# Kernel optimization log

Measured on AMD Instinct MI355X. Metric: run time of the kernel, lower is better.

Reference implementation:

```python
import jax, jax.numpy as jnp
import numpy as np

N = 10000   # nodes
E = 100000  # edges (before self-loops)
H = 4       # heads (layers 0-3); last layer uses 1 head
C = 200     # out_channels per head
IN_DIMS = [200, H * C, H * C, H * C, H * C]
HEADS   = [H, H, H, H, 1]
NEG_SLOPE = 0.2  # PyG GATConv default


def _gat_layer(x, src, dst, W, a_src, a_dst, b, heads):
    # x: [N, Fin], W: [Fin, heads*C], a_src/a_dst: [heads, C], b: [heads*C]
    h = (x @ W).reshape(N, heads, C)                       # [N,H,C]
    alpha_src = jnp.einsum('nhc,hc->nh', h, a_src)         # [N,H]
    alpha_dst = jnp.einsum('nhc,hc->nh', h, a_dst)         # [N,H]
    e = jax.nn.leaky_relu(alpha_src[src] + alpha_dst[dst], NEG_SLOPE)  # [E',H]
    # segment softmax over incoming edges of each dst node
    m = jax.ops.segment_max(e, dst, num_segments=N)        # [N,H]
    ex = jnp.exp(e - m[dst])                               # [E',H]
    den = jax.ops.segment_sum(ex, dst, num_segments=N)     # [N,H]
    alpha = ex / den[dst]                                  # [E',H]
    out = jax.ops.segment_sum(h[src] * alpha[:, :, None], dst, num_segments=N)
    return out.reshape(N, heads * C) + b, alpha


def setup_inputs() -> dict:
    key = jax.random.key(0)
    ks = jax.random.split(key, 2 + 4 * 5)
    inp = {}
    inp['X'] = jax.random.normal(ks[0], (N, 200), jnp.float32)
    inp['edge_index'] = jax.random.randint(ks[1], (2, E), 0, N, dtype=jnp.int32)
    k = 2
    for i in range(5):
        fin, hd = IN_DIMS[i], HEADS[i]
        s = 1.0 / np.sqrt(fin)
        inp[f'W{i}'] = jax.random.normal(ks[k], (fin, hd * C), jnp.float32) * s; k += 1
        inp[f'as{i}'] = jax.random.normal(ks[k], (hd, C), jnp.float32) * s; k += 1
        inp[f'ad{i}'] = jax.random.normal(ks[k], (hd, C), jnp.float32) * s; k += 1
        inp[f'b{i}'] = jnp.zeros((hd * C,), jnp.float32); k += 1
    return inp


def reference(X, edge_index,
              W0, as0, ad0, b0, W1, as1, ad1, b1, W2, as2, ad2, b2,
              W3, as3, ad3, b3, W4, as4, ad4, b4):
    # add self-loops (PyG GATConv default add_self_loops=True)
    loops = jnp.arange(N, dtype=edge_index.dtype)
    src = jnp.concatenate([edge_index[0], loops])
    dst = jnp.concatenate([edge_index[1], loops])
    gelu = lambda v: jax.nn.gelu(v, approximate=False)
    # eval mode: all dropouts are identity
    x, _ = _gat_layer(X, src, dst, W0, as0, ad0, b0, HEADS[0]); x = gelu(x)
    x, _ = _gat_layer(x, src, dst, W1, as1, ad1, b1, HEADS[1]); x = gelu(x)
    x, _ = _gat_layer(x, src, dst, W2, as2, ad2, b2, HEADS[2]); x = gelu(x)
    x, _ = _gat_layer(x, src, dst, W3, as3, ad3, b3, HEADS[3]); x = gelu(x)
    x, edge_attn = _gat_layer(x, src, dst, W4, as4, ad4, b4, HEADS[4])
    x = gelu(x)
    return (x, edge_attn)
```

## Files before the change

kernel.cpp:

```cpp
#include <hip/hip_runtime.h>
#include <math.h>

#define NN 10000
#define EE 100000
#define EPE 110000
#define CC 200
#define MPAD 10112

typedef __attribute__((ext_vector_type(8))) _Float16 f16x8;
typedef __attribute__((ext_vector_type(4))) _Float16 f16x4;
typedef __attribute__((ext_vector_type(4))) unsigned short u16x4;
typedef __attribute__((ext_vector_type(4))) float f32x4;

__device__ __forceinline__ float lrelu(float v) { return v >= 0.f ? v : 0.2f * v; }
__device__ __forceinline__ float gelu_f(float v) { return 0.5f * v * (1.f + erff(v * 0.70710678118654752f)); }


__global__ void build_edges_kernel(const int* __restrict__ ei,
                                   int* __restrict__ src_all, int* __restrict__ dst_all,
                                   int* __restrict__ deg) {
    int e = blockIdx.x * blockDim.x + threadIdx.x;
    if (e >= EPE) return;
    int s, d;
    if (e < EE) { s = ei[e]; d = ei[EE + e]; }
    else        { s = e - EE; d = e - EE; }
    src_all[e] = s;
    dst_all[e] = d;
    atomicAdd(&deg[d], 1);
}

__global__ void scan_kernel(const int* __restrict__ deg, int* __restrict__ row_ptr) {
    int tid = threadIdx.x;
    int lane = tid & 63, w = tid >> 6;
    int base = tid * 10;
    int v[10];
    int tot = 0;
#pragma unroll
    for (int j = 0; j < 10; ++j) {
        int idx = base + j;
        v[j] = (idx < NN) ? deg[idx] : 0;
        tot += v[j];
    }
    int inc = tot;
#pragma unroll
    for (int off = 1; off < 64; off <<= 1) {
        int t = __shfl_up(inc, off);
        if (lane >= off) inc += t;
    }
    __shared__ int ws[16];
    if (lane == 63) ws[w] = inc;
    __syncthreads();
    if (w == 0) {
        int s = (lane < 16) ? ws[lane] : 0;
#pragma unroll
        for (int off = 1; off < 16; off <<= 1) {
            int t = __shfl_up(s, off);
            if (lane >= off) s += t;
        }
        if (lane < 16) ws[lane] = s;
    }
    __syncthreads();
    int excl = inc - tot + ((w > 0) ? ws[w - 1] : 0);
    int run = excl;
#pragma unroll
    for (int j = 0; j < 10; ++j) {
        int idx = base + j;
        if (idx < NN) row_ptr[idx] = run;
        run += v[j];
    }
    if (base == NN) row_ptr[NN] = excl;
}

__global__ void scatter_kernel(const int* __restrict__ src_all, const int* __restrict__ dst_all,
                               const int* __restrict__ row_ptr, int* __restrict__ cursor,
                               int* __restrict__ col_src, int* __restrict__ col_eid) {
    int e = blockIdx.x * blockDim.x + threadIdx.x;
    if (e >= EPE) return;
    int d = dst_all[e];
    int pos = row_ptr[d] + atomicAdd(&cursor[d], 1);
    col_src[pos] = src_all[e];
    col_eid[pos] = e;
}


#define PREP_R0 79
#define PREP_R1 (PREP_R0 + 1614)
#define PREP_R2 (PREP_R1 + 10112)
#define PREP_R3 (PREP_R2 + 2616)

__global__ __launch_bounds__(256) void prep_kernel(const float* __restrict__ X,
                                                   const float* __restrict__ W0,
                                                   const float* __restrict__ W1,
                                                   const float* __restrict__ W2,
                                                   const float* __restrict__ W3,
                                                   const float* __restrict__ W4,
                                                   int* __restrict__ degcur,
                                                   unsigned short* __restrict__ Ap0,
                                                   unsigned short* __restrict__ Ap,
                                                   unsigned short* __restrict__ Bp) {
    __shared__ float tl[32][33];
    int bid = blockIdx.x;
    int tid = threadIdx.x;

    if (bid < PREP_R0) {
        int idx = bid * 256 + tid;
        if (idx < 2 * NN) degcur[idx] = 0;
        return;
    }
    if (bid < PREP_R1) {
        int idx = (bid - PREP_R0) * 256 + tid;
        if (idx < NN * 32) {
            int rw = idx >> 5, c = idx & 31;
            Ap[(size_t)rw * 832 + 800 + c] = 0;
        } else {
            int j = idx - NN * 32;
            if (j < (MPAD - NN) * 832) {
                int rw = j / 832, c = j - rw * 832;
                Ap[(size_t)(NN + rw) * 832 + c] = 0;
            }
        }
        return;
    }
    if (bid < PREP_R2) {
        int idx = (bid - PREP_R1) * 256 + tid;
        int row = idx >> 8, kk = idx & 255;
        float v = 0.f;
        if (row < NN && kk < 200) v = X[(size_t)row * 200 + kk];
        Ap0[idx] = __builtin_bit_cast(unsigned short, (_Float16)v);
        return;
    }
    int t = bid - PREP_R2;
    int l, t0;
    if (t < 224)       { l = 0; t0 = 0; }
    else if (t < 952)  { l = 1; t0 = 224; }
    else if (t < 1680) { l = 2; t0 = 952; }
    else if (t < 2408) { l = 3; t0 = 1680; }
    else               { l = 4; t0 = 2408; }
    const float* W = (l == 0) ? W0 : (l == 1) ? W1 : (l == 2) ? W2 : (l == 3) ? W3 : W4;
    int Fin = (l == 0) ? 200 : 800;
    int HC  = (l == 4) ? 200 : 800;
    int Kp  = (l == 0) ? 256 : 832;
    int ntk = Kp >> 5;
    int tile = t - t0;
    int kt = tile % ntk, nt = tile / ntk;
    int n0 = nt * 32, k0 = kt * 32;
    int tx = tid & 31, ty = tid >> 5;

#pragma unroll
    for (int j = 0; j < 4; ++j) {
        int kk = k0 + ty + j * 8;
        int n  = n0 + tx;
        float v = (kk < Fin && n < HC) ? W[(size_t)kk * HC + n] : 0.f;
        tl[ty + j * 8][tx] = v;
    }
    __syncthreads();
    unsigned short* Bpl = Bp + (size_t)l * (896 * 832);
#pragma unroll
    for (int j = 0; j < 4; ++j) {
        int n  = n0 + ty + j * 8;
        int kk = k0 + tx;
        Bpl[(size_t)n * Kp + kk] =
            __builtin_bit_cast(unsigned short, (_Float16)tl[tx][ty + j * 8]);
    }
}


__global__ __launch_bounds__(256) void gemm_mfma(const unsigned short* __restrict__ A,
                                                 const unsigned short* __restrict__ B,
                                                 unsigned short* __restrict__ C,
                                                 int Kt, int Np, int ncol) {
    __shared__ unsigned short As[8192];
    __shared__ unsigned short Bs[8192];

    int tid = threadIdx.x;
    int lane = tid & 63, wave = tid >> 6;

    int nwg = gridDim.x;
    int orig = blockIdx.x;
    int q = nwg >> 3, r = nwg & 7;
    int xcd = orig & 7, sidx = orig >> 3;
    int wg = (xcd < r ? xcd * (q + 1) : r * (q + 1) + (xcd - r) * q) + sidx;
    int rowT = wg / ncol, colT = wg - rowT * ncol;
    int row0 = rowT * 128, col0 = colT * 128;
    int wr = wave >> 1, wc = wave & 1;

    size_t gAoff[4], gBoff[4];
    int ldsSeg[4];
#pragma unroll
    for (int i = 0; i < 4; ++i) {
        int seg = wave * 4 + i;
        int chunkIdx = seg * 64 + lane;
        int rr = chunkIdx >> 3;
        int c = chunkIdx & 7;
        int cg = c ^ (rr & 7);
        gAoff[i] = (size_t)(row0 + rr) * Kt + (size_t)cg * 8;
        gBoff[i] = (size_t)(col0 + rr) * Kt + (size_t)cg * 8;
        ldsSeg[i] = seg * 512;
    }

    int rowA[4], rowB[4];
#pragma unroll
    for (int m = 0; m < 4; ++m) {
        rowA[m] = wr * 64 + m * 16 + (lane & 15);
        rowB[m] = wc * 64 + m * 16 + (lane & 15);
    }

    int iaOff[2][4], ibOff[2][4];
#pragma unroll
    for (int kh = 0; kh < 2; ++kh) {
        int cw = kh * 4 + (lane >> 4);
#pragma unroll
        for (int m = 0; m < 4; ++m)
            iaOff[kh][m] = rowA[m] * 64 + ((cw ^ (rowA[m] & 7)) << 3);
#pragma unroll
        for (int n = 0; n < 4; ++n)
            ibOff[kh][n] = rowB[n] * 64 + ((cw ^ (rowB[n] & 7)) << 3);
    }

    f32x4 acc[4][4];
#pragma unroll
    for (int m = 0; m < 4; ++m)
#pragma unroll
        for (int n = 0; n < 4; ++n) acc[m][n] = f32x4{0.f, 0.f, 0.f, 0.f};

    for (int k0 = 0; k0 < Kt; k0 += 64) {
#pragma unroll
        for (int i = 0; i < 4; ++i) {
            __builtin_amdgcn_global_load_lds(
                (const __attribute__((address_space(1))) void*)(A + gAoff[i] + k0),
                (__attribute__((address_space(3))) void*)(&As[ldsSeg[i]]), 16, 0, 0);
            __builtin_amdgcn_global_load_lds(
                (const __attribute__((address_space(1))) void*)(B + gBoff[i] + k0),
                (__attribute__((address_space(3))) void*)(&Bs[ldsSeg[i]]), 16, 0, 0);
        }
        __syncthreads();

#pragma unroll
        for (int kh = 0; kh < 2; ++kh) {
            f16x8 a[4], b[4];
#pragma unroll
            for (int m = 0; m < 4; ++m) a[m] = *(const f16x8*)(&As[iaOff[kh][m]]);
#pragma unroll
            for (int n = 0; n < 4; ++n) b[n] = *(const f16x8*)(&Bs[ibOff[kh][n]]);
#pragma unroll
            for (int m = 0; m < 4; ++m)
#pragma unroll
                for (int n = 0; n < 4; ++n)
                    acc[m][n] = __builtin_amdgcn_mfma_f32_16x16x32_f16(a[m], b[n], acc[m][n], 0, 0, 0);
        }
        __syncthreads();
    }

    int crow = row0 + wr * 64 + ((lane >> 4) << 2);
    int ccol = col0 + wc * 64 + (lane & 15);
#pragma unroll
    for (int m = 0; m < 4; ++m)
#pragma unroll
        for (int j = 0; j < 4; ++j) {
            size_t rb = (size_t)(crow + m * 16 + j) * Np;
#pragma unroll
            for (int n = 0; n < 4; ++n)
                C[rb + ccol + n * 16] =
                    __builtin_bit_cast(unsigned short, (_Float16)acc[m][n][j]);
        }
}


__global__ void attn_kernel(const unsigned short* __restrict__ h,
                            const float* __restrict__ a_s, const float* __restrict__ a_d,
                            float* __restrict__ asrc, float* __restrict__ adst,
                            int H, int HCp) {
    int n = blockIdx.x;
    int wave = threadIdx.x >> 6;
    int lane = threadIdx.x & 63;
    float sa = 0.f, da = 0.f;
    int c0 = lane * 4;
    if (c0 < CC) {
        f16x4 hv = *(const f16x4*)(h + (size_t)n * HCp + wave * CC + c0);
        float4 av = *(const float4*)(a_s + wave * CC + c0);
        float4 dv = *(const float4*)(a_d + wave * CC + c0);
        float h0 = (float)hv[0], h1 = (float)hv[1], h2 = (float)hv[2], h3 = (float)hv[3];
        sa = h0 * av.x + h1 * av.y + h2 * av.z + h3 * av.w;
        da = h0 * dv.x + h1 * dv.y + h2 * dv.z + h3 * dv.w;
    }
#pragma unroll
    for (int off = 32; off > 0; off >>= 1) {
        sa += __shfl_down(sa, off);
        da += __shfl_down(da, off);
    }
    if (lane == 0) {
        asrc[n * H + wave] = sa;
        adst[n * H + wave] = da;
    }
}


__global__ __launch_bounds__(256) void fused_agg_kernel(const unsigned short* __restrict__ h,
                                                        const float* __restrict__ asrc,
                                                        const float* __restrict__ adst,
                                                        const int* __restrict__ row_ptr,
                                                        const int* __restrict__ col_src,
                                                        const int* __restrict__ col_eid,
                                                        const float* __restrict__ bias,
                                                        float* __restrict__ out32,
                                                        unsigned short* __restrict__ apn,
                                                        float* __restrict__ wout,
                                                        int H, int HC, int HCp) {
    int n = blockIdx.x;
    int tid = threadIdx.x;
    int wave = tid >> 6, lane = tid & 63;
    int beg = row_ptr[n], end = row_ptr[n + 1];

    __shared__ float m_s[4], inv_s[4], ad_s[4];
    __shared__ float w_lds[64 * 4];
    __shared__ int src_lds[64];

    if (wave < H) {
        float ad = adst[n * H + wave];
        float m = -1e30f, den = 0.f;
        for (int e = beg + lane; e < end; e += 64) {
            float v = lrelu(asrc[col_src[e] * H + wave] + ad);
            if (v > m) { den = den * expf(m - v) + 1.f; m = v; }
            else den += expf(v - m);
        }
#pragma unroll
        for (int off = 1; off < 64; off <<= 1) {
            float m2 = __shfl_xor(m, off);
            float d2 = __shfl_xor(den, off);
            float M = fmaxf(m, m2);
            den = den * expf(m - M) + d2 * expf(m2 - M);
            m = M;
        }
        if (lane == 0) { m_s[wave] = m; inv_s[wave] = 1.f / den; ad_s[wave] = ad; }
    }
    __syncthreads();

    int ch0 = tid * 4;
    int head = ch0 / CC;
    float a0 = 0.f, a1 = 0.f, a2 = 0.f, a3 = 0.f;

    for (int c0 = beg; c0 < end; c0 += 64) {
        int cnt = min(64, end - c0);
        if (wave < H && lane < cnt) {
            int e = c0 + lane;
            int s = col_src[e];
            float v = lrelu(asrc[s * H + wave] + ad_s[wave]);
            float wv = expf(v - m_s[wave]) * inv_s[wave];
            w_lds[lane * 4 + wave] = wv;
            if (wave == 0) src_lds[lane] = s;
            if (wout) wout[(size_t)col_eid[e] * H + wave] = wv;
        }
        __syncthreads();
        if (ch0 < HC) {
            f16x4 hva = {}, hvb = {};
            hva = *(const f16x4*)(h + (size_t)src_lds[0] * HCp + ch0);
            if (cnt > 1) hvb = *(const f16x4*)(h + (size_t)src_lds[1] * HCp + ch0);
            for (int j = 0; j < cnt; ++j) {
                f16x4 hvc = {};
                if (j + 2 < cnt) hvc = *(const f16x4*)(h + (size_t)src_lds[j + 2] * HCp + ch0);
                float wv = w_lds[j * 4 + head];
                a0 += wv * (float)hva[0];
                a1 += wv * (float)hva[1];
                a2 += wv * (float)hva[2];
                a3 += wv * (float)hva[3];
                hva = hvb; hvb = hvc;
            }
        }
        __syncthreads();
    }

    if (ch0 < HC) {
        float4 bv = *(const float4*)(bias + ch0);
        float g0 = gelu_f(a0 + bv.x), g1 = gelu_f(a1 + bv.y);
        float g2 = gelu_f(a2 + bv.z), g3 = gelu_f(a3 + bv.w);
        if (out32) {
            *(float4*)(out32 + (size_t)n * HC + ch0) = float4{g0, g1, g2, g3};
        } else {
            *(u16x4*)(apn + (size_t)n * 832 + ch0) = u16x4{
                __builtin_bit_cast(unsigned short, (_Float16)g0),
                __builtin_bit_cast(unsigned short, (_Float16)g1),
                __builtin_bit_cast(unsigned short, (_Float16)g2),
                __builtin_bit_cast(unsigned short, (_Float16)g3)};
        }
    }
}


extern "C" void kernel_launch(void* const* d_in, const int* in_sizes, int n_in,
                              void* d_out, int out_size, void* d_ws, size_t ws_size,
                              hipStream_t stream) {
    const float* X = (const float*)d_in[0];
    const int* ei = (const int*)d_in[1];

    char* ws = (char*)d_ws;
    size_t off = 0;
    auto alloc = [&](size_t bytes) { void* p = ws + off; off += (bytes + 255) & ~(size_t)255; return p; };

    unsigned short* Ap0 = (unsigned short*)alloc((size_t)MPAD * 256 * 2);
    unsigned short* Ap  = (unsigned short*)alloc((size_t)MPAD * 832 * 2);
    unsigned short* Bp  = (unsigned short*)alloc((size_t)5 * 896 * 832 * 2);
    unsigned short* hbuf= (unsigned short*)alloc((size_t)MPAD * 896 * 2);
    float* attn_all = (float*)alloc((size_t)5 * 2 * NN * 4 * 4);
    int* src_all  = (int*)alloc((size_t)EPE * 4);
    int* dst_all  = (int*)alloc((size_t)EPE * 4);
    int* col_src  = (int*)alloc((size_t)EPE * 4);
    int* col_eid  = (int*)alloc((size_t)EPE * 4);
    int* row_ptr  = (int*)alloc((size_t)(NN + 1) * 4);
    int* degcur   = (int*)alloc((size_t)2 * NN * 4);
    int* deg = degcur, * cursor = degcur + NN;

    prep_kernel<<<PREP_R3, 256, 0, stream>>>(X,
        (const float*)d_in[2], (const float*)d_in[6], (const float*)d_in[10],
        (const float*)d_in[14], (const float*)d_in[18],
        degcur, Ap0, Ap, Bp);

    int eb = (EPE + 255) / 256;
    build_edges_kernel<<<eb, 256, 0, stream>>>(ei, src_all, dst_all, deg);
    scan_kernel<<<1, 1024, 0, stream>>>(deg, row_ptr);
    scatter_kernel<<<eb, 256, 0, stream>>>(src_all, dst_all, row_ptr, cursor, col_src, col_eid);

    for (int i = 0; i < 5; ++i) {
        int H   = (i == 4) ? 1 : 4;
        int HC  = H * CC;
        int Kp  = (i == 0) ? 256 : 832;
        int Np  = (i == 4) ? 256 : 896;
        int ncol = Np / 128;
        const unsigned short* Acur = (i == 0) ? Ap0 : Ap;
        const unsigned short* Bpl = Bp + (size_t)i * (896 * 832);
        const float* as_ = (const float*)d_in[3 + 4 * i];
        const float* ad_ = (const float*)d_in[4 + 4 * i];
        const float* b_  = (const float*)d_in[5 + 4 * i];
        float* asrc_l = attn_all + (size_t)i * 2 * NN * 4;
        float* adst_l = asrc_l + NN * 4;

        gemm_mfma<<<ncol * (MPAD / 128), 256, 0, stream>>>(Acur, Bpl, hbuf, Kp, Np, ncol);

        attn_kernel<<<NN, H * 64, 0, stream>>>(hbuf, as_, ad_, asrc_l, adst_l, H, Np);

        float* out32 = (i == 4) ? (float*)d_out : nullptr;
        unsigned short* apn = (i == 4) ? nullptr : Ap;
        float* wout = (i == 4) ? (float*)d_out + (size_t)NN * CC : nullptr;
        fused_agg_kernel<<<NN, 256, 0, stream>>>(hbuf, asrc_l, adst_l, row_ptr, col_src,
                                                 col_eid, b_, out32, apn, wout, H, HC, Np);
    }
}
```

Before: 441.8 us.

## Make aggregation wave-per-head with shuffles instead of LDS and block barriers

The aggregation kernel now assigns one wavefront to each head. Each wave computes its own softmax statistics and broadcasts edge weights and source indices through lane shuffles, which removes the shared-memory staging and the __syncthreads barriers. The block size becomes H*64, so the last layer launches a single wave per node. In exchange only 50 of 64 lanes carry channels, since 200 channels at 4 per lane leaves 14 lanes idle, and each wave repeats the per-edge loads on its own.

```diff
diff --git a/kernel.cpp b/kernel.cpp
--- a/kernel.cpp
+++ b/kernel.cpp
@@ -295,88 +295,84 @@
 }
 
 
-__global__ __launch_bounds__(256) void fused_agg_kernel(const unsigned short* __restrict__ h,
-                                                        const float* __restrict__ asrc,
-                                                        const float* __restrict__ adst,
-                                                        const int* __restrict__ row_ptr,
-                                                        const int* __restrict__ col_src,
-                                                        const int* __restrict__ col_eid,
-                                                        const float* __restrict__ bias,
-                                                        float* __restrict__ out32,
-                                                        unsigned short* __restrict__ apn,
-                                                        float* __restrict__ wout,
-                                                        int H, int HC, int HCp) {
+__global__ void fused_agg_kernel(const unsigned short* __restrict__ h,
+                                 const float* __restrict__ asrc,
+                                 const float* __restrict__ adst,
+                                 const int* __restrict__ row_ptr,
+                                 const int* __restrict__ col_src,
+                                 const int* __restrict__ col_eid,
+                                 const float* __restrict__ bias,
+                                 float* __restrict__ out32,
+                                 unsigned short* __restrict__ apn,
+                                 float* __restrict__ wout,
+                                 int H, int HC, int HCp) {
     int n = blockIdx.x;
-    int tid = threadIdx.x;
-    int wave = tid >> 6, lane = tid & 63;
+    int head = threadIdx.x >> 6;
+    int lane = threadIdx.x & 63;
     int beg = row_ptr[n], end = row_ptr[n + 1];
 
-    __shared__ float m_s[4], inv_s[4], ad_s[4];
-    __shared__ float w_lds[64 * 4];
-    __shared__ int src_lds[64];
-
-    if (wave < H) {
-        float ad = adst[n * H + wave];
-        float m = -1e30f, den = 0.f;
-        for (int e = beg + lane; e < end; e += 64) {
-            float v = lrelu(asrc[col_src[e] * H + wave] + ad);
-            if (v > m) { den = den * expf(m - v) + 1.f; m = v; }
-            else den += expf(v - m);
-        }
-#pragma unroll
-        for (int off = 1; off < 64; off <<= 1) {
-            float m2 = __shfl_xor(m, off);
-            float d2 = __shfl_xor(den, off);
-            float M = fmaxf(m, m2);
-            den = den * expf(m - M) + d2 * expf(m2 - M);
-            m = M;
-        }
-        if (lane == 0) { m_s[wave] = m; inv_s[wave] = 1.f / den; ad_s[wave] = ad; }
-    }
-    __syncthreads();
-
-    int ch0 = tid * 4;
-    int head = ch0 / CC;
+    float ad = adst[n * H + head];
+
+    float m = -1e30f, den = 0.f;
+    for (int e = beg + lane; e < end; e += 64) {
+        float v = lrelu(asrc[col_src[e] * H + head] + ad);
+        if (v > m) { den = den * expf(m - v) + 1.f; m = v; }
+        else den += expf(v - m);
+    }
+#pragma unroll
+    for (int off = 1; off < 64; off <<= 1) {
+        float m2 = __shfl_xor(m, off);
+        float d2 = __shfl_xor(den, off);
+        float M = fmaxf(m, m2);
+        den = den * expf(m - M) + d2 * expf(m2 - M);
+        m = M;
+    }
+    float inv = 1.f / den;
+
+    int c4 = lane * 4;
+    bool own = (c4 < CC);
+    const unsigned short* hbase = h + (size_t)head * CC + c4;
     float a0 = 0.f, a1 = 0.f, a2 = 0.f, a3 = 0.f;
 
     for (int c0 = beg; c0 < end; c0 += 64) {
         int cnt = min(64, end - c0);
-        if (wave < H && lane < cnt) {
+        int s = 0; float wv = 0.f;
+        if (lane < cnt) {
             int e = c0 + lane;
-            int s = col_src[e];
-            float v = lrelu(asrc[s * H + wave] + ad_s[wave]);
-            float wv = expf(v - m_s[wave]) * inv_s[wave];
-            w_lds[lane * 4 + wave] = wv;
-            if (wave == 0) src_lds[lane] = s;
-            if (wout) wout[(size_t)col_eid[e] * H + wave] = wv;
-        }
-        __syncthreads();
-        if (ch0 < HC) {
-            f16x4 hva = {}, hvb = {};
-            hva = *(const f16x4*)(h + (size_t)src_lds[0] * HCp + ch0);
-            if (cnt > 1) hvb = *(const f16x4*)(h + (size_t)src_lds[1] * HCp + ch0);
-            for (int j = 0; j < cnt; ++j) {
-                f16x4 hvc = {};
-                if (j + 2 < cnt) hvc = *(const f16x4*)(h + (size_t)src_lds[j + 2] * HCp + ch0);
-                float wv = w_lds[j * 4 + head];
-                a0 += wv * (float)hva[0];
-                a1 += wv * (float)hva[1];
-                a2 += wv * (float)hva[2];
-                a3 += wv * (float)hva[3];
-                hva = hvb; hvb = hvc;
-            }
-        }
-        __syncthreads();
-    }
-
-    if (ch0 < HC) {
-        float4 bv = *(const float4*)(bias + ch0);
+            s = col_src[e];
+            float v = lrelu(asrc[s * H + head] + ad);
+            wv = expf(v - m) * inv;
+            if (wout) wout[(size_t)col_eid[e] * H + head] = wv;
+        }
+        int sj0 = __shfl(s, 0);
+        int sj1 = __shfl(s, (cnt > 1) ? 1 : 0);
+        f16x4 hva = {}, hvb = {};
+        if (own) {
+            hva = *(const f16x4*)(hbase + (size_t)sj0 * HCp);
+            if (cnt > 1) hvb = *(const f16x4*)(hbase + (size_t)sj1 * HCp);
+        }
+        for (int j = 0; j < cnt; ++j) {
+            int sj2 = __shfl(s, (j + 2 < cnt) ? j + 2 : 0);
+            float wj = __shfl(wv, j);
+            f16x4 hvc = {};
+            if (own && j + 2 < cnt) hvc = *(const f16x4*)(hbase + (size_t)sj2 * HCp);
+            a0 += wj * (float)hva[0];
+            a1 += wj * (float)hva[1];
+            a2 += wj * (float)hva[2];
+            a3 += wj * (float)hva[3];
+            hva = hvb; hvb = hvc;
+        }
+    }
+
+    if (own) {
+        int ch = head * CC + c4;
+        float4 bv = *(const float4*)(bias + ch);
         float g0 = gelu_f(a0 + bv.x), g1 = gelu_f(a1 + bv.y);
         float g2 = gelu_f(a2 + bv.z), g3 = gelu_f(a3 + bv.w);
         if (out32) {
-            *(float4*)(out32 + (size_t)n * HC + ch0) = float4{g0, g1, g2, g3};
+            *(float4*)(out32 + (size_t)n * HC + ch) = float4{g0, g1, g2, g3};
         } else {
-            *(u16x4*)(apn + (size_t)n * 832 + ch0) = u16x4{
+            *(u16x4*)(apn + (size_t)n * 832 + ch) = u16x4{
                 __builtin_bit_cast(unsigned short, (_Float16)g0),
                 __builtin_bit_cast(unsigned short, (_Float16)g1),
                 __builtin_bit_cast(unsigned short, (_Float16)g2),
@@ -440,7 +436,7 @@
         float* out32 = (i == 4) ? (float*)d_out : nullptr;
         unsigned short* apn = (i == 4) ? nullptr : Ap;
         float* wout = (i == 4) ? (float*)d_out + (size_t)NN * CC : nullptr;
-        fused_agg_kernel<<<NN, 256, 0, stream>>>(hbuf, asrc_l, adst_l, row_ptr, col_src,
-                                                 col_eid, b_, out32, apn, wout, H, HC, Np);
-    }
-}
+        fused_agg_kernel<<<NN, H * 64, 0, stream>>>(hbuf, asrc_l, adst_l, row_ptr, col_src,
+                                                    col_eid, b_, out32, apn, wout, H, HC, Np);
+    }
+}
```

Result: slower. 469.6 us (+6.3%).
